# Kernel optimization log

Hardware: AMD Instinct MI355X
Metric: run time of the kernel (lower is better)

The kernel has to match this reference:

```python
import jax, jax.numpy as jnp
import numpy as np
from jax import lax

# BinarizedConv2d (threshold=False branch): per-direction binary conv.
# Bits {0,1} map to {-1,+1}; output = 2*A - K where A = #bit-agreements
# between the patch and the filter, K = Cin*kH*kW (the 'offset').
# A = 2*sum(x&w) - sum(x) - sum(w) + K  =>  out = 4*xw - 2*sx - 2*sw + K.

D, H, W, CIN = 64, 32, 32, 128
KH = KW = 3
COUT = 128
PAD = 1


def _binconv(x, w):
    # x: [D,H,W,Cin] bool, w: [D,kH,kW,Cin,Cout] with 0/1 float values
    d, h, wd, c = x.shape
    kh, kw, cout = w.shape[1], w.shape[2], w.shape[4]
    K = c * kh * kw  # offset = in_channels * kH * kW
    xf = jnp.transpose(x.astype(w.dtype), (0, 3, 1, 2))  # [D,C,H,W]
    # im2col: [D, C*kH*kW, Ho, Wo], feature index = c*kH*kW + i*kW + j
    patches = lax.conv_general_dilated_patches(
        xf, (kh, kw), (1, 1), [(PAD, PAD), (PAD, PAD)])
    ho, wo = patches.shape[2], patches.shape[3]
    p = patches.reshape(d, c, kh, kw, ho, wo)
    xw = jnp.einsum('dcijhw,dijco->dhwo', p, w)      # sum(x & w)
    sx = p.sum(axis=(1, 2, 3))                        # [D,Ho,Wo]
    sw = w.sum(axis=(1, 2, 3))                        # [D,Cout]
    return 4.0 * xw - 2.0 * sx[..., None] - 2.0 * sw[:, None, None, :] + K


def setup_inputs() -> dict:
    key = jax.random.key(0)
    kx, kw = jax.random.split(key)
    x = jax.random.bernoulli(kx, 0.5, (D, H, W, CIN))
    w = jax.random.bernoulli(kw, 0.5, (D, KH, KW, CIN, COUT)).astype(jnp.float32)
    return {'x': x, 'w': w}


def reference(x, w):
    return _binconv(x, w)  # [D,Ho,Wo,Cout] signed binary conv values
```

## Files before the change

kernel.cpp:

```cpp
#include <hip/hip_runtime.h>
#include <stdint.h>


#define D_    64
#define H_    32
#define W_    32
#define CIN_  128
#define COUT_ 128
#define KK_   1152

__global__ __launch_bounds__(1024) void fused_kernel(const int* __restrict__ x,
                                                     const float* __restrict__ w,
                                                     float* __restrict__ out) {
    __shared__ uint4    xbt[10][34];
    __shared__ unsigned wt[128][40];

    int tid  = threadIdx.x;
    int bid  = blockIdx.x;
    int d    = bid & 63;
    int tile = bid >> 6;
    int h0   = tile * 8;

    if (tid < 20) {
        int r = tid >> 1, c = (tid & 1) ? 33 : 0;
        xbt[r][c] = make_uint4(0u, 0u, 0u, 0u);
    }

    const int* xd = x + (long)d * (H_ * W_ * CIN_);
#pragma unroll
    for (int it = 0; it < 10; ++it) {
        int t   = tid + it * 1024;
        int c4  = t & 31;
        int pl  = t >> 5;
        int r   = pl >> 5;
        int col = pl & 31;
        int hh  = h0 - 1 + r;
        int4 v = make_int4(0, 0, 0, 0);
        if (hh >= 0 && hh < H_)
            v = ((const int4*)(xd + (long)(hh * W_ + col) * CIN_))[c4];
        unsigned long long b0 = __ballot(v.x != 0);
        unsigned long long b1 = __ballot(v.y != 0);
        unsigned long long b2 = __ballot(v.z != 0);
        unsigned long long b3 = __ballot(v.w != 0);
        int lane = tid & 63;
        if (lane == 0)
            xbt[r][col + 1] = make_uint4((unsigned)b0, (unsigned)b1,
                                         (unsigned)b2, (unsigned)b3);
        else if (lane == 32)
            xbt[r][col + 1] = make_uint4((unsigned)(b0 >> 32), (unsigned)(b1 >> 32),
                                         (unsigned)(b2 >> 32), (unsigned)(b3 >> 32));
    }

    const float* wd = w + (long)d * (9 * CIN_ * COUT_);
    for (int t = tid; t < 4608; t += 1024) {
        int o    = t & 127;
        int rest = t >> 7;
        int tap  = rest >> 2;
        int k    = rest & 3;
        const float* wp = wd + (long)tap * (CIN_ * COUT_) + o;
        unsigned m = 0;
#pragma unroll
        for (int j = 0; j < 32; ++j)
            if (wp[(long)(4 * j + k) * COUT_] != 0.f) m |= 1u << j;
        wt[o][rest] = m;
    }

    __syncthreads();

    int o   = tid & 127;
    int grp = tid >> 7;

    uint4 wv[9];
#pragma unroll
    for (int t = 0; t < 9; ++t)
        wv[t] = *(const uint4*)&wt[o][t * 4];

    int h = h0 + grp;
    float* op = out + ((long)d * (H_ * W_) + h * W_) * COUT_ + o;

    uint4 ca[3], cb[3], cc_[3];
#pragma unroll
    for (int i = 0; i < 3; ++i) {
        ca[i] = xbt[grp + i][0];
        cb[i] = xbt[grp + i][1];
    }

#pragma unroll
    for (int iw = 0; iw < W_; ++iw) {
#pragma unroll
        for (int i = 0; i < 3; ++i) cc_[i] = xbt[grp + i][iw + 2];
        int pop = 0;
#pragma unroll
        for (int i = 0; i < 3; ++i) {
            uint4 xa;
            uint4 w0 = wv[i * 3 + 0], w1 = wv[i * 3 + 1], w2 = wv[i * 3 + 2];
            xa = ca[i];
            pop += __popc(xa.x ^ w0.x) + __popc(xa.y ^ w0.y)
                 + __popc(xa.z ^ w0.z) + __popc(xa.w ^ w0.w);
            xa = cb[i];
            pop += __popc(xa.x ^ w1.x) + __popc(xa.y ^ w1.y)
                 + __popc(xa.z ^ w1.z) + __popc(xa.w ^ w1.w);
            xa = cc_[i];
            pop += __popc(xa.x ^ w2.x) + __popc(xa.y ^ w2.y)
                 + __popc(xa.z ^ w2.z) + __popc(xa.w ^ w2.w);
        }
        op[(long)iw * COUT_] = (float)(KK_ - 2 * pop);
#pragma unroll
        for (int i = 0; i < 3; ++i) { ca[i] = cb[i]; cb[i] = cc_[i]; }
    }
}

extern "C" void kernel_launch(void* const* d_in, const int* in_sizes, int n_in,
                              void* d_out, int out_size, void* d_ws, size_t ws_size,
                              hipStream_t stream) {
    const int*   x   = (const int*)d_in[0];
    const float* w   = (const float*)d_in[1];
    float*       out = (float*)d_out;
    (void)d_ws; (void)ws_size;

    fused_kernel<<<256, 1024, 0, stream>>>(x, w, out);
}
```

Baseline: 130.7 us.

## Split into global bit-pack kernel and fine-grained conv kernel via workspace

Packing the input and weights into bitmasks moves from a per-block shared-memory prologue into a separate grid-wide kernel that writes to the workspace buffer. A second kernel, launched with 2048 small blocks (one per depth and row), reads the packed bits from global memory and computes the XOR-popcount convolution. The aim is better parallelism and occupancy than 256 blocks of 1024 threads, and no longer redoing the weight packing inside each row tile. The cost is an extra launch, a global round trip for the packed data, and uncoalesced strided weight loads in the pack kernel. The old fused kernel remains as a fallback when the workspace is too small.

New measurement: 127.1 us. 2.8% less time.

```diff
diff --git a/kernel.cpp b/kernel.cpp
--- a/kernel.cpp
+++ b/kernel.cpp
@@ -8,6 +8,118 @@
 #define CIN_  128
 #define COUT_ 128
 #define KK_   1152
+
+#define XPK_ROWS 34
+#define XPK_N    (D_ * XPK_ROWS * W_)
+#define WPK_N    (D_ * 36 * COUT_)
+
+__global__ __launch_bounds__(256) void pack_kernel(const int* __restrict__ x,
+                                                   const float* __restrict__ w,
+                                                   uint4* __restrict__ xpk,
+                                                   unsigned* __restrict__ wpk) {
+    int tid = blockIdx.x * 256 + threadIdx.x;
+    int nth = gridDim.x * 256;
+
+    for (int t = tid; t < D_ * 2 * W_; t += nth) {
+        int d = t >> 6;
+        int r = (t & 32) ? (XPK_ROWS - 1) : 0;
+        int c = t & 31;
+        xpk[(d * XPK_ROWS + r) * W_ + c] = make_uint4(0u, 0u, 0u, 0u);
+    }
+
+    int lane   = threadIdx.x & 63;
+    int wave   = tid >> 6;
+    int nwaves = nth >> 6;
+    for (int wt = wave; wt < (D_ * H_ * W_) / 2; wt += nwaves) {
+        int p  = wt * 2;
+        int d  = p >> 10;
+        int h  = (p >> 5) & 31;
+        int c0 = p & 31;
+        const int* xp = x + (long)p * CIN_ + ((lane >> 5) ? CIN_ : 0);
+        int4 v = ((const int4*)xp)[lane & 31];
+        unsigned long long b0 = __ballot(v.x != 0);
+        unsigned long long b1 = __ballot(v.y != 0);
+        unsigned long long b2 = __ballot(v.z != 0);
+        unsigned long long b3 = __ballot(v.w != 0);
+        if (lane == 0)
+            xpk[(d * XPK_ROWS + h + 1) * W_ + c0] =
+                make_uint4((unsigned)b0, (unsigned)b1, (unsigned)b2, (unsigned)b3);
+        else if (lane == 32)
+            xpk[(d * XPK_ROWS + h + 1) * W_ + c0 + 1] =
+                make_uint4((unsigned)(b0 >> 32), (unsigned)(b1 >> 32),
+                           (unsigned)(b2 >> 32), (unsigned)(b3 >> 32));
+    }
+
+    for (int t = tid; t < WPK_N; t += nth) {
+        int o    = t & 127;
+        int dr   = t >> 7;
+        int rest = dr % 36;
+        int d    = dr / 36;
+        int tap  = rest >> 2;
+        int k    = rest & 3;
+        const float* wp = w + ((long)d * 9 + tap) * (CIN_ * COUT_) + o;
+        unsigned m = 0;
+#pragma unroll
+        for (int j = 0; j < 32; ++j)
+            if (wp[(long)(4 * j + k) * COUT_] != 0.f) m |= 1u << j;
+        wpk[t] = m;
+    }
+}
+
+__global__ __launch_bounds__(128) void conv_kernel(const uint4* __restrict__ xpk,
+                                                   const unsigned* __restrict__ wpk,
+                                                   float* __restrict__ out) {
+    int bid = blockIdx.x;
+    int d   = bid >> 5;
+    int h   = bid & 31;
+    int o   = threadIdx.x;
+
+    const unsigned* wb = wpk + (long)d * 36 * COUT_ + o;
+    uint4 wv[9];
+#pragma unroll
+    for (int t = 0; t < 9; ++t) {
+        wv[t].x = wb[(t * 4 + 0) * COUT_];
+        wv[t].y = wb[(t * 4 + 1) * COUT_];
+        wv[t].z = wb[(t * 4 + 2) * COUT_];
+        wv[t].w = wb[(t * 4 + 3) * COUT_];
+    }
+
+    const uint4* xp = xpk + ((long)d * XPK_ROWS + h) * W_;
+    float* op = out + ((long)(d * H_ + h) * W_) * COUT_ + o;
+
+    uint4 ca[3], cb[3], cc_[3];
+#pragma unroll
+    for (int i = 0; i < 3; ++i) {
+        ca[i] = make_uint4(0u, 0u, 0u, 0u);
+        cb[i] = xp[i * W_];
+    }
+
+#pragma unroll
+    for (int iw = 0; iw < W_; ++iw) {
+#pragma unroll
+        for (int i = 0; i < 3; ++i)
+            cc_[i] = (iw < W_ - 1) ? xp[i * W_ + iw + 1]
+                                   : make_uint4(0u, 0u, 0u, 0u);
+        int pop = 0;
+#pragma unroll
+        for (int i = 0; i < 3; ++i) {
+            uint4 xa;
+            uint4 w0 = wv[i * 3 + 0], w1 = wv[i * 3 + 1], w2 = wv[i * 3 + 2];
+            xa = ca[i];
+            pop += __popc(xa.x ^ w0.x) + __popc(xa.y ^ w0.y)
+                 + __popc(xa.z ^ w0.z) + __popc(xa.w ^ w0.w);
+            xa = cb[i];
+            pop += __popc(xa.x ^ w1.x) + __popc(xa.y ^ w1.y)
+                 + __popc(xa.z ^ w1.z) + __popc(xa.w ^ w1.w);
+            xa = cc_[i];
+            pop += __popc(xa.x ^ w2.x) + __popc(xa.y ^ w2.y)
+                 + __popc(xa.z ^ w2.z) + __popc(xa.w ^ w2.w);
+        }
+        op[(long)iw * COUT_] = (float)(KK_ - 2 * pop);
+#pragma unroll
+        for (int i = 0; i < 3; ++i) { ca[i] = cb[i]; cb[i] = cc_[i]; }
+    }
+}
 
 __global__ __launch_bounds__(1024) void fused_kernel(const int* __restrict__ x,
                                                      const float* __restrict__ w,
@@ -116,7 +228,14 @@
     const int*   x   = (const int*)d_in[0];
     const float* w   = (const float*)d_in[1];
     float*       out = (float*)d_out;
-    (void)d_ws; (void)ws_size;
-
-    fused_kernel<<<256, 1024, 0, stream>>>(x, w, out);
-}
+
+    size_t need = (size_t)XPK_N * 16 + (size_t)WPK_N * 4;
+    if (d_ws && ws_size >= need) {
+        uint4*    xpk = (uint4*)d_ws;
+        unsigned* wpk = (unsigned*)((char*)d_ws + (size_t)XPK_N * 16);
+        pack_kernel<<<1024, 256, 0, stream>>>(x, w, xpk, wpk);
+        conv_kernel<<<2048, 128, 0, stream>>>(xpk, wpk, out);
+    } else {
+        fused_kernel<<<256, 1024, 0, stream>>>(x, w, out);
+    }
+}
```

## Split bit-packing into a separate kernel and run the conv on packed global buffers

Applied to the files above, without the earlier changes.

Replaces the single fused kernel (256 blocks of 1024 threads) with a pack kernel that bit-packs x and w once into global device buffers, followed by a conv kernel with 2048 blocks of 128 threads, one row per block. The fused version repacked the full weight set of a depth slice in every block (4 blocks per d), so weights were packed four times over. The new layout removes that redundancy and raises the block count. The cost is a second launch and a round trip through global memory for the packed data, and the conv kernel now reads x bits straight from global memory instead of shared memory.

Result: faster. 126.8 us (-3.0%).

```diff
diff --git a/kernel.cpp b/kernel.cpp
--- a/kernel.cpp
+++ b/kernel.cpp
@@ -9,86 +9,96 @@
 #define COUT_ 128
 #define KK_   1152
 
-__global__ __launch_bounds__(1024) void fused_kernel(const int* __restrict__ x,
-                                                     const float* __restrict__ w,
-                                                     float* __restrict__ out) {
-    __shared__ uint4    xbt[10][34];
-    __shared__ unsigned wt[128][40];
+#define XPK_ROWS 34
+#define XPK_N    (D_ * XPK_ROWS * W_)
+#define WPK_N    (D_ * 36 * COUT_)
 
-    int tid  = threadIdx.x;
-    int bid  = blockIdx.x;
-    int d    = bid & 63;
-    int tile = bid >> 6;
-    int h0   = tile * 8;
+__device__ uint4    g_xpk[XPK_N];
+__device__ unsigned g_wpk[WPK_N];
 
-    if (tid < 20) {
-        int r = tid >> 1, c = (tid & 1) ? 33 : 0;
-        xbt[r][c] = make_uint4(0u, 0u, 0u, 0u);
+__global__ __launch_bounds__(256) void pack_kernel(const int* __restrict__ x,
+                                                   const float* __restrict__ w) {
+    int tid = blockIdx.x * 256 + threadIdx.x;
+    int nth = gridDim.x * 256;
+
+    for (int t = tid; t < D_ * 2 * W_; t += nth) {
+        int d = t >> 6;
+        int r = (t & 32) ? (XPK_ROWS - 1) : 0;
+        int c = t & 31;
+        g_xpk[(d * XPK_ROWS + r) * W_ + c] = make_uint4(0u, 0u, 0u, 0u);
     }
 
-    const int* xd = x + (long)d * (H_ * W_ * CIN_);
-#pragma unroll
-    for (int it = 0; it < 10; ++it) {
-        int t   = tid + it * 1024;
-        int c4  = t & 31;
-        int pl  = t >> 5;
-        int r   = pl >> 5;
-        int col = pl & 31;
-        int hh  = h0 - 1 + r;
-        int4 v = make_int4(0, 0, 0, 0);
-        if (hh >= 0 && hh < H_)
-            v = ((const int4*)(xd + (long)(hh * W_ + col) * CIN_))[c4];
+    int lane   = threadIdx.x & 63;
+    int wave   = tid >> 6;
+    int nwaves = nth >> 6;
+    for (int wt = wave; wt < (D_ * H_ * W_) / 2; wt += nwaves) {
+        int p  = wt * 2;
+        int d  = p >> 10;
+        int h  = (p >> 5) & 31;
+        int c0 = p & 31;
+        const int* xp = x + (long)p * CIN_ + ((lane >> 5) ? CIN_ : 0);
+        int4 v = ((const int4*)xp)[lane & 31];
         unsigned long long b0 = __ballot(v.x != 0);
         unsigned long long b1 = __ballot(v.y != 0);
         unsigned long long b2 = __ballot(v.z != 0);
         unsigned long long b3 = __ballot(v.w != 0);
-        int lane = tid & 63;
         if (lane == 0)
-            xbt[r][col + 1] = make_uint4((unsigned)b0, (unsigned)b1,
-                                         (unsigned)b2, (unsigned)b3);
+            g_xpk[(d * XPK_ROWS + h + 1) * W_ + c0] =
+                make_uint4((unsigned)b0, (unsigned)b1, (unsigned)b2, (unsigned)b3);
         else if (lane == 32)
-            xbt[r][col + 1] = make_uint4((unsigned)(b0 >> 32), (unsigned)(b1 >> 32),
-                                         (unsigned)(b2 >> 32), (unsigned)(b3 >> 32));
+            g_xpk[(d * XPK_ROWS + h + 1) * W_ + c0 + 1] =
+                make_uint4((unsigned)(b0 >> 32), (unsigned)(b1 >> 32),
+                           (unsigned)(b2 >> 32), (unsigned)(b3 >> 32));
     }
 
-    const float* wd = w + (long)d * (9 * CIN_ * COUT_);
-    for (int t = tid; t < 4608; t += 1024) {
+    for (int t = tid; t < WPK_N; t += nth) {
         int o    = t & 127;
-        int rest = t >> 7;
+        int dr   = t >> 7;
+        int rest = dr % 36;
+        int d    = dr / 36;
         int tap  = rest >> 2;
         int k    = rest & 3;
-        const float* wp = wd + (long)tap * (CIN_ * COUT_) + o;
+        const float* wp = w + ((long)d * 9 + tap) * (CIN_ * COUT_) + o;
         unsigned m = 0;
 #pragma unroll
         for (int j = 0; j < 32; ++j)
             if (wp[(long)(4 * j + k) * COUT_] != 0.f) m |= 1u << j;
-        wt[o][rest] = m;
+        g_wpk[t] = m;
+    }
+}
+
+__global__ __launch_bounds__(128) void conv_kernel(float* __restrict__ out) {
+    int bid = blockIdx.x;
+    int d   = bid >> 5;
+    int h   = bid & 31;
+    int o   = threadIdx.x;
+
+    const unsigned* wb = g_wpk + (long)d * 36 * COUT_ + o;
+    uint4 wv[9];
+#pragma unroll
+    for (int t = 0; t < 9; ++t) {
+        wv[t].x = wb[(t * 4 + 0) * COUT_];
+        wv[t].y = wb[(t * 4 + 1) * COUT_];
+        wv[t].z = wb[(t * 4 + 2) * COUT_];
+        wv[t].w = wb[(t * 4 + 3) * COUT_];
     }
 
-    __syncthreads();
-
-    int o   = tid & 127;
-    int grp = tid >> 7;
-
-    uint4 wv[9];
-#pragma unroll
-    for (int t = 0; t < 9; ++t)
-        wv[t] = *(const uint4*)&wt[o][t * 4];
-
-    int h = h0 + grp;
-    float* op = out + ((long)d * (H_ * W_) + h * W_) * COUT_ + o;
+    const uint4* xp = g_xpk + ((long)d * XPK_ROWS + h) * W_;
+    float* op = out + ((long)(d * H_ + h) * W_) * COUT_ + o;
 
     uint4 ca[3], cb[3], cc_[3];
 #pragma unroll
     for (int i = 0; i < 3; ++i) {
-        ca[i] = xbt[grp + i][0];
-        cb[i] = xbt[grp + i][1];
+        ca[i] = make_uint4(0u, 0u, 0u, 0u);
+        cb[i] = xp[i * W_];
     }
 
 #pragma unroll
     for (int iw = 0; iw < W_; ++iw) {
 #pragma unroll
-        for (int i = 0; i < 3; ++i) cc_[i] = xbt[grp + i][iw + 2];
+        for (int i = 0; i < 3; ++i)
+            cc_[i] = (iw < W_ - 1) ? xp[i * W_ + iw + 1]
+                                   : make_uint4(0u, 0u, 0u, 0u);
         int pop = 0;
 #pragma unroll
         for (int i = 0; i < 3; ++i) {
@@ -118,5 +128,6 @@
     float*       out = (float*)d_out;
     (void)d_ws; (void)ws_size;
 
-    fused_kernel<<<256, 1024, 0, stream>>>(x, w, out);
+    pack_kernel<<<1024, 256, 0, stream>>>(x, w);
+    conv_kernel<<<2048, 128, 0, stream>>>(out);
 }
```
